# Kernel tuning notes

Hardware: AMD Instinct MI355X
Metric: run time of the kernel (lower is better)

## Reference

```python
import jax, jax.numpy as jnp
import numpy as np

C = 512
NH = 8
HD = C // NH
GROUPS = 8
EPS = 1e-5

def group_norm(x, w, b):
    # x: [B,C,H,W], 8 groups
    B, Cc, H, W = x.shape
    xg = x.reshape(B, GROUPS, Cc // GROUPS, H, W)
    mu = xg.mean(axis=(2, 3, 4), keepdims=True)
    var = xg.var(axis=(2, 3, 4), keepdims=True)
    xn = (xg - mu) * jax.lax.rsqrt(var + EPS)
    xn = xn.reshape(B, Cc, H, W)
    return xn * w[None, :, None, None] + b[None, :, None, None]

def conv1x1(x, w, b):
    # w: [O,C], b: [O]
    return jnp.einsum('oc,bchw->bohw', w, x) + b[None, :, None, None]

def setup_inputs() -> dict:
    key = jax.random.key(0)
    ks = jax.random.split(key, 12)
    s = 1.0 / np.sqrt(C)
    inp = {
        'x': jax.random.normal(ks[0], (8, C, 32, 32), dtype=jnp.float32),
        'norm_w': jnp.ones((C,), jnp.float32),
        'norm_b': jnp.zeros((C,), jnp.float32),
        'qw': jax.random.uniform(ks[1], (C, C), jnp.float32, -s, s),
        'qb': jax.random.uniform(ks[2], (C,), jnp.float32, -s, s),
        'kw': jax.random.uniform(ks[3], (C, C), jnp.float32, -s, s),
        'kb': jax.random.uniform(ks[4], (C,), jnp.float32, -s, s),
        'vw': jax.random.uniform(ks[5], (C, C), jnp.float32, -s, s),
        'vb': jax.random.uniform(ks[6], (C,), jnp.float32, -s, s),
        'pw': jax.random.uniform(ks[7], (C, C), jnp.float32, -s, s),
        'pb': jax.random.uniform(ks[8], (C,), jnp.float32, -s, s),
    }
    return inp

def reference(x, norm_w, norm_b, qw, qb, kw, kb, vw, vb, pw, pb):
    b, c, h, w = x.shape
    scale = HD ** (-0.5)
    xn = group_norm(x, norm_w, norm_b)
    q = conv1x1(xn, qw, qb).reshape(b, NH, HD, h * w)
    k = conv1x1(xn, kw, kb).reshape(b, NH, HD, h * w)
    v = conv1x1(xn, vw, vb).reshape(b, NH, HD, h * w)
    attn = jnp.einsum('bhcn,bhcm->bhnm', q, k) * scale
    attn = jax.nn.softmax(attn, axis=-1)
    out = jnp.einsum('bhnm,bhcm->bhcn', attn, v)
    out = out.reshape(b, c, h, w)
    out = conv1x1(out, pw, pb)
    return out + x
```

## Files before the change

kernel.cpp:

```cpp
#include <hip/hip_runtime.h>

#define C_DIM 512
#define N_PIX 1024
#define B_DIM 8
#define NHEAD 8
#define HDIM 64
#define NGRP 8
#define CG 64
#define EPSF 1e-5f

typedef __bf16 bf16x8_t __attribute__((ext_vector_type(8)));
typedef __bf16 bf16x4_t __attribute__((ext_vector_type(4)));
typedef float  f32x4_t  __attribute__((ext_vector_type(4)));
typedef unsigned int u32x4_t __attribute__((ext_vector_type(4)));

__device__ __forceinline__ __bf16 f2b(float f) {
  unsigned int u = __builtin_bit_cast(unsigned int, f);
  u += 0x7fffu + ((u >> 16) & 1u);
  unsigned short s = (unsigned short)(u >> 16);
  return __builtin_bit_cast(__bf16, s);
}

__device__ __forceinline__ unsigned int pack_trunc(float a, float b) {
  return (__builtin_bit_cast(unsigned int, a) >> 16) |
         (__builtin_bit_cast(unsigned int, b) & 0xffff0000u);
}

__device__ __forceinline__ void async16(const void* g, void* l) {
  __builtin_amdgcn_global_load_lds((const __attribute__((address_space(1))) void*)g,
                                   (__attribute__((address_space(3))) void*)l, 16, 0, 0);
}

__global__ __launch_bounds__(256) void prep_kernel(
    const float* __restrict__ qw, const float* __restrict__ kw,
    const float* __restrict__ vw, const float* __restrict__ pw,
    __bf16* __restrict__ wb,
    const float* __restrict__ x, float2* __restrict__ psum)
{
  if (blockIdx.x < 1024) {
    int idx = blockIdx.x * 256 + threadIdx.x;
    int mat = idx >> 16;
    int off = (idx & 65535) * 4;
    const float* src = (mat == 0) ? qw : (mat == 1) ? kw : (mat == 2) ? vw : pw;
    float4 v = *(const float4*)(src + off);
    bf16x4_t pk;
    pk[0] = f2b(v.x); pk[1] = f2b(v.y); pk[2] = f2b(v.z); pk[3] = f2b(v.w);
    *(bf16x4_t*)(wb + mat * (512 * 512) + off) = pk;
  } else {
    const int t = blockIdx.x - 1024;
    const int s = t & 7, bg = t >> 3;
    const float* xp = x + ((size_t)bg * CG + s * 8) * N_PIX;
    float sum = 0.f, sum2 = 0.f;
#pragma unroll
    for (int it = 0; it < 8; it++) {
      float4 v = ((const float4*)xp)[it * 256 + threadIdx.x];
      sum  += v.x + v.y + v.z + v.w;
      sum2 += v.x * v.x + v.y * v.y + v.z * v.z + v.w * v.w;
    }
#pragma unroll
    for (int off = 32; off; off >>= 1) {
      sum  += __shfl_xor(sum, off, 64);
      sum2 += __shfl_xor(sum2, off, 64);
    }
    __shared__ float red[8];
    const int lane = threadIdx.x & 63, wv = threadIdx.x >> 6;
    if (lane == 0) { red[wv] = sum; red[4 + wv] = sum2; }
    __syncthreads();
    if (threadIdx.x == 0) {
      float s1 = red[0] + red[1] + red[2] + red[3];
      float s2 = red[4] + red[5] + red[6] + red[7];
      psum[bg * 8 + s] = make_float2(s1, s2);
    }
  }
}

__global__ __launch_bounds__(256) void gn_apply_kernel(
    const float* __restrict__ x, const float2* __restrict__ psum,
    const float* __restrict__ gw, const float* __restrict__ gb,
    __bf16* __restrict__ xnT)
{
  const int n0 = blockIdx.x * 32, b = blockIdx.y;
  const int tid = threadIdx.x;
  __shared__ float mu_s[8], rs_s[8];
  __shared__ __align__(16) __bf16 tile[32 * 520];

  if (tid < 8) {
    float s1 = 0.f, s2 = 0.f;
#pragma unroll
    for (int i = 0; i < 8; i++) {
      float2 p = psum[(b * 8 + tid) * 8 + i];
      s1 += p.x; s2 += p.y;
    }
    const float inv = 1.f / (float)(CG * N_PIX);
    float mu = s1 * inv;
    float var = s2 * inv - mu * mu;
    mu_s[tid] = mu;
    rs_s[tid] = rsqrtf(var + EPSF);
  }
  __syncthreads();

  const float* xb = x + (size_t)b * C_DIM * N_PIX + n0;
  const int cl = tid >> 3;
  const int nq = (tid & 7) * 4;
#pragma unroll
  for (int co = 0; co < 16; co++) {
    const int c = co * 32 + cl;
    float4 v = *(const float4*)(xb + (size_t)c * N_PIX + nq);
    const int g = c >> 6;
    const float rs = rs_s[g];
    const float a = rs * gw[c];
    const float bb = gb[c] - mu_s[g] * a;
    tile[(nq + 0) * 520 + c] = f2b(v.x * a + bb);
    tile[(nq + 1) * 520 + c] = f2b(v.y * a + bb);
    tile[(nq + 2) * 520 + c] = f2b(v.z * a + bb);
    tile[(nq + 3) * 520 + c] = f2b(v.w * a + bb);
  }
  __syncthreads();

  __bf16* dst = xnT + ((size_t)b * N_PIX + n0) * C_DIM;
  const int l32 = tid & 31, nr = tid >> 5;
#pragma unroll
  for (int no = 0; no < 4; no++) {
    const int n = no * 8 + nr;
#pragma unroll
    for (int co = 0; co < 2; co++) {
      const int c = co * 256 + l32 * 8;
      *(bf16x8_t*)(dst + (size_t)n * C_DIM + c) =
          *(const bf16x8_t*)(tile + n * 520 + c);
    }
  }
}

__device__ __forceinline__ void gemm_core_64(
    const __bf16* __restrict__ A, const __bf16* __restrict__ B,
    __bf16* As, __bf16* Bs, f32x4_t acc[2][4])
{
  const int tid  = threadIdx.x;
  const int lane = tid & 63;
  const int wv   = tid >> 6;
  const int quad = lane >> 4;
  const int l16  = lane & 15;
  const int wm = (wv >> 1) * 32;
  const int wn = (wv & 1) * 64;

  f32x4_t zero = {0.f, 0.f, 0.f, 0.f};
#pragma unroll
  for (int i = 0; i < 2; i++)
#pragma unroll
    for (int j = 0; j < 4; j++) acc[i][j] = zero;

  const int chA  = wv * 64 + lane;
  const int rA = chA >> 2,  kA = (chA & 3) * 8;
  const int chB0 = wv * 64 + lane, chB1 = 256 + wv * 64 + lane;
  const int rB0 = chB0 >> 2, kB0 = (chB0 & 3) * 8;
  const int rB1 = chB1 >> 2, kB1 = (chB1 & 3) * 8;

  for (int kt = 0; kt < 512; kt += 64) {
#pragma unroll
    for (int p = 0; p < 2; p++) {
      async16(A + (size_t)rA * 512 + kt + p * 32 + kA,  As + p * 2048 + (wv * 64) * 8);
      async16(B + (size_t)rB0 * 512 + kt + p * 32 + kB0, Bs + p * 4096 + (wv * 64) * 8);
      async16(B + (size_t)rB1 * 512 + kt + p * 32 + kB1, Bs + p * 4096 + (256 + wv * 64) * 8);
    }
    __builtin_amdgcn_s_waitcnt(0);
    __syncthreads();
#pragma unroll
    for (int p = 0; p < 2; p++) {
      bf16x8_t af[2], bfr[4];
#pragma unroll
      for (int i = 0; i < 2; i++)
        af[i] = *(const bf16x8_t*)(As + p * 2048 + (wm + i * 16 + l16) * 32 + quad * 8);
#pragma unroll
      for (int j = 0; j < 4; j++)
        bfr[j] = *(const bf16x8_t*)(Bs + p * 4096 + (wn + j * 16 + l16) * 32 + quad * 8);
#pragma unroll
      for (int i = 0; i < 2; i++)
#pragma unroll
        for (int j = 0; j < 4; j++)
          acc[i][j] = __builtin_amdgcn_mfma_f32_16x16x32_bf16(af[i], bfr[j], acc[i][j], 0, 0, 0);
    }
    __syncthreads();
  }
}

__global__ __launch_bounds__(256, 4) void gemm_qkv_kernel(
    const __bf16* __restrict__ wqkv, const float* __restrict__ qb,
    const float* __restrict__ kb, const float* __restrict__ vb,
    const __bf16* __restrict__ xnT,
    __bf16* __restrict__ qT, __bf16* __restrict__ kT, __bf16* __restrict__ vbuf)
{
  __shared__ __align__(16) __bf16 smem[12288];
  __bf16* As = smem;
  __bf16* Bs = smem + 4096;
  const int b = blockIdx.x;
  const int n0 = blockIdx.y * 128;
  const int z = blockIdx.z;
  const int mat = z >> 3;
  const int m0 = (z & 7) * 64;
  const __bf16* A = wqkv + (size_t)mat * (512 * 512) + (size_t)m0 * 512;
  const __bf16* B = xnT + ((size_t)b * N_PIX + n0) * 512;
  f32x4_t acc[2][4];
  gemm_core_64(A, B, As, Bs, acc);

  const int tid = threadIdx.x, lane = tid & 63, wv = tid >> 6;
  const int quad = lane >> 4, l16 = lane & 15;
  const int wm = (wv >> 1) * 32, wn = (wv & 1) * 64;
  const float* bias = (mat == 0) ? qb : (mat == 1) ? kb : vb;
  const float qscale = (mat == 0) ? 0.125f * 1.44269504f : 1.0f;

  if (mat < 2) {
    __bf16* dst = (mat == 0) ? qT : kT;
#pragma unroll
    for (int i = 0; i < 2; i++) {
      const int crow = wm + i * 16 + quad * 4;
      const int o = m0 + crow;
      float b0 = bias[o], b1 = bias[o + 1], b2 = bias[o + 2], b3 = bias[o + 3];
#pragma unroll
      for (int j = 0; j < 4; j++) {
        const int nl = wn + j * 16 + l16;
        bf16x4_t pk;
        pk[0] = f2b((acc[i][j][0] + b0) * qscale);
        pk[1] = f2b((acc[i][j][1] + b1) * qscale);
        pk[2] = f2b((acc[i][j][2] + b2) * qscale);
        pk[3] = f2b((acc[i][j][3] + b3) * qscale);
        *(bf16x4_t*)(smem + nl * 72 + crow) = pk;
      }
    }
    __syncthreads();
#pragma unroll
    for (int it = 0; it < 4; it++) {
      const int n = it * 32 + (tid >> 3);
      const int c = (tid & 7) * 8;
      *(bf16x8_t*)(dst + ((size_t)b * N_PIX + n0 + n) * 512 + m0 + c) =
          *(const bf16x8_t*)(smem + n * 72 + c);
    }
  } else {
#pragma unroll
    for (int i = 0; i < 2; i++) {
      const int crow = wm + i * 16 + quad * 4;
      const int o = m0 + crow;
      float b0 = bias[o], b1 = bias[o + 1], b2 = bias[o + 2], b3 = bias[o + 3];
#pragma unroll
      for (int j = 0; j < 4; j++) {
        const int nl = wn + j * 16 + l16;
        smem[(crow + 0) * 132 + nl] = f2b(acc[i][j][0] + b0);
        smem[(crow + 1) * 132 + nl] = f2b(acc[i][j][1] + b1);
        smem[(crow + 2) * 132 + nl] = f2b(acc[i][j][2] + b2);
        smem[(crow + 3) * 132 + nl] = f2b(acc[i][j][3] + b3);
      }
    }
    __syncthreads();
    const int c = tid >> 2;
    const int nch = (tid & 3) * 32;
    __bf16* vd = vbuf + ((size_t)b * 512 + m0 + c) * N_PIX + n0 + nch;
#pragma unroll
    for (int k = 0; k < 4; k++)
      *(bf16x8_t*)(vd + k * 8) = *(const bf16x8_t*)(smem + c * 132 + nch + k * 8);
  }
}

__global__ __launch_bounds__(256, 2) void attn_kernel(
    const __bf16* __restrict__ qT, const __bf16* __restrict__ kT,
    const __bf16* __restrict__ vbuf, __bf16* __restrict__ aT)
{
  __shared__ __align__(16) __bf16 Ks[2][64 * 72];
  __shared__ __align__(16) __bf16 Vp[2][64 * 72];
  const int bh = blockIdx.x;
  const int b = bh >> 3, head = bh & 7;
  const int n0 = blockIdx.y * 128;
  const int tid = threadIdx.x, lane = tid & 63, wv = tid >> 6;
  const int quad = lane >> 4, l16 = lane & 15;

  bf16x8_t qf[2][2];
#pragma unroll
  for (int qt = 0; qt < 2; qt++) {
    const __bf16* qp = qT + ((size_t)b * N_PIX + n0 + wv * 32 + qt * 16 + l16) * 512 + head * 64;
    qf[qt][0] = *(const bf16x8_t*)(qp + quad * 8);
    qf[qt][1] = *(const bf16x8_t*)(qp + 32 + quad * 8);
  }

  const __bf16* kp = kT + ((size_t)b * N_PIX) * 512 + head * 64;
  const __bf16* vp = vbuf + ((size_t)b * 512 + head * 64) * N_PIX;

  const int srow = tid >> 2, scol = (tid & 3) * 16;
  const int pr0 = scol >> 5, hh0 = (scol >> 4) & 1;
  const int pos0 = pr0 * 32 + ((scol >> 2) & 3) * 8 + hh0 * 4;
  const int mc1 = scol + 8;
  const int pr1 = mc1 >> 5, hh1 = (mc1 >> 4) & 1;
  const int pos1 = pr1 * 32 + ((mc1 >> 2) & 3) * 8 + hh1 * 4;

  bf16x8_t kreg0 = *(const bf16x8_t*)(kp + (size_t)srow * 512 + scol);
  bf16x8_t kreg1 = *(const bf16x8_t*)(kp + (size_t)srow * 512 + scol + 8);
  bf16x8_t vreg0 = *(const bf16x8_t*)(vp + (size_t)srow * N_PIX + scol);
  bf16x8_t vreg1 = *(const bf16x8_t*)(vp + (size_t)srow * N_PIX + scol + 8);
  {
    *(bf16x8_t*)(Ks[0] + srow * 72 + scol)     = kreg0;
    *(bf16x8_t*)(Ks[0] + srow * 72 + scol + 8) = kreg1;
    bf16x4_t lo, hi;
#pragma unroll
    for (int r = 0; r < 4; r++) { lo[r] = vreg0[r]; hi[r] = vreg0[4 + r]; }
    *(bf16x4_t*)(Vp[0] + srow * 72 + pos0)     = lo;
    *(bf16x4_t*)(Vp[0] + srow * 72 + pos0 + 8) = hi;
#pragma unroll
    for (int r = 0; r < 4; r++) { lo[r] = vreg1[r]; hi[r] = vreg1[4 + r]; }
    *(bf16x4_t*)(Vp[0] + srow * 72 + pos1)     = lo;
    *(bf16x4_t*)(Vp[0] + srow * 72 + pos1 + 8) = hi;
  }
  kreg0 = *(const bf16x8_t*)(kp + (size_t)(64 + srow) * 512 + scol);
  kreg1 = *(const bf16x8_t*)(kp + (size_t)(64 + srow) * 512 + scol + 8);
  vreg0 = *(const bf16x8_t*)(vp + (size_t)srow * N_PIX + 64 + scol);
  vreg1 = *(const bf16x8_t*)(vp + (size_t)srow * N_PIX + 64 + scol + 8);
  __syncthreads();

  const f32x4_t zero = {0.f, 0.f, 0.f, 0.f};
  f32x4_t oacc[2][4];
#pragma unroll
  for (int qt = 0; qt < 2; qt++)
#pragma unroll
    for (int jc = 0; jc < 4; jc++) oacc[qt][jc] = zero;
  f32x4_t lsum4[2] = {zero, zero};

  for (int mt = 0; mt < 16; mt++) {
    const int cur = mt & 1, nxt = cur ^ 1;
    const __bf16* Kc = Ks[cur];
    const __bf16* Vc = Vp[cur];

    f32x4_t sacc[2][4];
#pragma unroll
    for (int mb = 0; mb < 4; mb++) {
      bf16x8_t kf0 = *(const bf16x8_t*)(Kc + (mb * 16 + l16) * 72 + quad * 8);
      bf16x8_t kf1 = *(const bf16x8_t*)(Kc + (mb * 16 + l16) * 72 + 32 + quad * 8);
#pragma unroll
      for (int qt = 0; qt < 2; qt++) {
        f32x4_t s = zero;
        s = __builtin_amdgcn_mfma_f32_16x16x32_bf16(kf0, qf[qt][0], s, 0, 0, 0);
        s = __builtin_amdgcn_mfma_f32_16x16x32_bf16(kf1, qf[qt][1], s, 0, 0, 0);
        sacc[qt][mb] = s;
      }
    }

    bf16x8_t pf[2][2];
#pragma unroll
    for (int qt = 0; qt < 2; qt++) {
      float p[4][4];
#pragma unroll
      for (int mb = 0; mb < 4; mb++)
#pragma unroll
        for (int r = 0; r < 4; r++) {
          p[mb][r] = __builtin_amdgcn_exp2f(sacc[qt][mb][r]);
          lsum4[qt][r] += p[mb][r];
        }
#pragma unroll
      for (int pr = 0; pr < 2; pr++) {
        u32x4_t u;
        u[0] = pack_trunc(p[2 * pr][0],     p[2 * pr][1]);
        u[1] = pack_trunc(p[2 * pr][2],     p[2 * pr][3]);
        u[2] = pack_trunc(p[2 * pr + 1][0], p[2 * pr + 1][1]);
        u[3] = pack_trunc(p[2 * pr + 1][2], p[2 * pr + 1][3]);
        pf[qt][pr] = __builtin_bit_cast(bf16x8_t, u);
      }
    }

#pragma unroll
    for (int jc = 0; jc < 4; jc++) {
      const int vrow = (jc * 16 + l16) * 72;
#pragma unroll
      for (int pr = 0; pr < 2; pr++) {
        bf16x8_t vf = *(const bf16x8_t*)(Vc + vrow + pr * 32 + quad * 8);
#pragma unroll
        for (int qt = 0; qt < 2; qt++)
          oacc[qt][jc] = __builtin_amdgcn_mfma_f32_16x16x32_bf16(vf, pf[qt][pr], oacc[qt][jc], 0, 0, 0);
      }
    }

    if (mt < 15) {
      *(bf16x8_t*)(Ks[nxt] + srow * 72 + scol)     = kreg0;
      *(bf16x8_t*)(Ks[nxt] + srow * 72 + scol + 8) = kreg1;
      bf16x4_t lo, hi;
#pragma unroll
      for (int r = 0; r < 4; r++) { lo[r] = vreg0[r]; hi[r] = vreg0[4 + r]; }
      *(bf16x4_t*)(Vp[nxt] + srow * 72 + pos0)     = lo;
      *(bf16x4_t*)(Vp[nxt] + srow * 72 + pos0 + 8) = hi;
#pragma unroll
      for (int r = 0; r < 4; r++) { lo[r] = vreg1[r]; hi[r] = vreg1[4 + r]; }
      *(bf16x4_t*)(Vp[nxt] + srow * 72 + pos1)     = lo;
      *(bf16x4_t*)(Vp[nxt] + srow * 72 + pos1 + 8) = hi;
      if (mt < 14) {
        kreg0 = *(const bf16x8_t*)(kp + (size_t)((mt + 2) * 64 + srow) * 512 + scol);
        kreg1 = *(const bf16x8_t*)(kp + (size_t)((mt + 2) * 64 + srow) * 512 + scol + 8);
        vreg0 = *(const bf16x8_t*)(vp + (size_t)srow * N_PIX + (mt + 2) * 64 + scol);
        vreg1 = *(const bf16x8_t*)(vp + (size_t)srow * N_PIX + (mt + 2) * 64 + scol + 8);
      }
      __syncthreads();
    }
  }

  __syncthreads();
  __bf16* Tr = &Ks[0][0];
#pragma unroll
  for (int qt = 0; qt < 2; qt++) {
    float lsum = lsum4[qt][0] + lsum4[qt][1] + lsum4[qt][2] + lsum4[qt][3];
    lsum += __shfl_xor(lsum, 16, 64);
    lsum += __shfl_xor(lsum, 32, 64);
    const float inv = 1.f / lsum;
    const int nl = wv * 32 + qt * 16 + l16;
#pragma unroll
    for (int jc = 0; jc < 4; jc++) {
      bf16x4_t o4;
#pragma unroll
      for (int r = 0; r < 4; r++) o4[r] = f2b(oacc[qt][jc][r] * inv);
      *(bf16x4_t*)(Tr + nl * 72 + jc * 16 + quad * 4) = o4;
    }
  }
  __syncthreads();
#pragma unroll
  for (int it = 0; it < 4; it++) {
    const int n = it * 32 + (tid >> 3);
    const int c = (tid & 7) * 8;
    *(bf16x8_t*)(aT + ((size_t)b * N_PIX + n0 + n) * 512 + head * 64 + c) =
        *(const bf16x8_t*)(Tr + n * 72 + c);
  }
}

__global__ __launch_bounds__(256, 4) void gemm_proj_kernel(
    const __bf16* __restrict__ wp, const float* __restrict__ pb,
    const __bf16* __restrict__ aT, const float* __restrict__ x,
    float* __restrict__ out)
{
  __shared__ __align__(16) __bf16 smem[12288];
  __bf16* As = smem;
  __bf16* Bs = smem + 4096;
  const int b = blockIdx.x;
  const int n0 = blockIdx.y * 128;
  const int m0 = blockIdx.z * 64;
  const __bf16* A = wp + (size_t)m0 * 512;
  const __bf16* B = aT + ((size_t)b * N_PIX + n0) * 512;
  f32x4_t acc[2][4];
  gemm_core_64(A, B, As, Bs, acc);
  const int tid = threadIdx.x, lane = tid & 63, wv = tid >> 6;
  const int quad = lane >> 4, l16 = lane & 15;
  const int wm = (wv >> 1) * 32, wn = (wv & 1) * 64;
#pragma unroll
  for (int i = 0; i < 2; i++) {
    const int o = m0 + wm + i * 16 + quad * 4;
#pragma unroll
    for (int j = 0; j < 4; j++) {
      const int n = n0 + wn + j * 16 + l16;
#pragma unroll
      for (int r = 0; r < 4; r++) {
        size_t idx = ((size_t)b * 512 + o + r) * N_PIX + n;
        out[idx] = acc[i][j][r] + pb[o + r] + x[idx];
      }
    }
  }
}

extern "C" void kernel_launch(void* const* d_in, const int* in_sizes, int n_in,
                              void* d_out, int out_size, void* d_ws, size_t ws_size,
                              hipStream_t stream)
{
  (void)in_sizes; (void)n_in; (void)out_size; (void)ws_size;
  const float* x   = (const float*)d_in[0];
  const float* gnw = (const float*)d_in[1];
  const float* gnb = (const float*)d_in[2];
  const float* qw  = (const float*)d_in[3];
  const float* qb  = (const float*)d_in[4];
  const float* kw  = (const float*)d_in[5];
  const float* kb  = (const float*)d_in[6];
  const float* vw  = (const float*)d_in[7];
  const float* vb  = (const float*)d_in[8];
  const float* pw  = (const float*)d_in[9];
  const float* pb  = (const float*)d_in[10];
  float* out = (float*)d_out;

  char* ws = (char*)d_ws;
  __bf16* wb   = (__bf16*)(ws);
  __bf16* xnT  = (__bf16*)(ws + (size_t)(2  << 20));
  __bf16* qTb  = (__bf16*)(ws + (size_t)(10 << 20));
  __bf16* kTb  = (__bf16*)(ws + (size_t)(18 << 20));
  __bf16* vbf  = (__bf16*)(ws + (size_t)(26 << 20));
  __bf16* aT   = (__bf16*)(ws + (size_t)(34 << 20));
  float2* psum = (float2*)(ws + (size_t)(42 << 20));

  hipLaunchKernelGGL(prep_kernel, dim3(1536), dim3(256), 0, stream,
                     qw, kw, vw, pw, wb, x, psum);
  hipLaunchKernelGGL(gn_apply_kernel, dim3(32, 8), dim3(256), 0, stream, x, psum, gnw, gnb, xnT);
  hipLaunchKernelGGL(gemm_qkv_kernel, dim3(8, 8, 24), dim3(256), 0, stream,
                     wb, qb, kb, vb, xnT, qTb, kTb, vbf);
  hipLaunchKernelGGL(attn_kernel, dim3(64, 8), dim3(256), 0, stream, qTb, kTb, vbf, aT);
  hipLaunchKernelGGL(gemm_proj_kernel, dim3(8, 8, 8), dim3(256), 0, stream,
                     wb + (size_t)3 * 512 * 512, pb, aT, x, out);
}
```

Before: 150.8 us.

## Fuse Q, K and V projections into one block sharing the activation tile

Each QKV GEMM block now computes the same 64-row output slice for all three weight matrices at once, so the xn activation tile is loaded once and reused across Q, K and V instead of being loaded three times by separate blocks. The grid shrinks from 1536 to 512 blocks, and each block holds three times the accumulators and a larger shared-memory buffer, with the occupancy bound lowered to 2. This cuts global and LDS traffic for the B operand but reduces parallelism to 512 blocks on a 256-CU device and raises register pressure.

```diff
diff --git a/kernel.cpp b/kernel.cpp
--- a/kernel.cpp
+++ b/kernel.cpp
@@ -183,32 +183,79 @@
   }
 }
 
-__global__ __launch_bounds__(256, 4) void gemm_qkv_kernel(
+__global__ __launch_bounds__(256, 2) void gemm_qkv_kernel(
     const __bf16* __restrict__ wqkv, const float* __restrict__ qb,
     const float* __restrict__ kb, const float* __restrict__ vb,
     const __bf16* __restrict__ xnT,
     __bf16* __restrict__ qT, __bf16* __restrict__ kT, __bf16* __restrict__ vbuf)
 {
-  __shared__ __align__(16) __bf16 smem[12288];
-  __bf16* As = smem;
-  __bf16* Bs = smem + 4096;
+  __shared__ __align__(16) __bf16 smem[20480];
+  __bf16* Bs = smem + 12288;
   const int b = blockIdx.x;
   const int n0 = blockIdx.y * 128;
-  const int z = blockIdx.z;
-  const int mat = z >> 3;
-  const int m0 = (z & 7) * 64;
-  const __bf16* A = wqkv + (size_t)mat * (512 * 512) + (size_t)m0 * 512;
-  const __bf16* B = xnT + ((size_t)b * N_PIX + n0) * 512;
-  f32x4_t acc[2][4];
-  gemm_core_64(A, B, As, Bs, acc);
+  const int m0 = blockIdx.z * 64;
+  const __bf16* Aq = wqkv + (size_t)m0 * 512;
+  const __bf16* Ak = Aq + 512 * 512;
+  const __bf16* Av = Ak + 512 * 512;
+  const __bf16* Bx = xnT + ((size_t)b * N_PIX + n0) * 512;
 
   const int tid = threadIdx.x, lane = tid & 63, wv = tid >> 6;
   const int quad = lane >> 4, l16 = lane & 15;
   const int wm = (wv >> 1) * 32, wn = (wv & 1) * 64;
-  const float* bias = (mat == 0) ? qb : (mat == 1) ? kb : vb;
-  const float qscale = (mat == 0) ? 0.125f * 1.44269504f : 1.0f;
-
-  if (mat < 2) {
+
+  const f32x4_t zero = {0.f, 0.f, 0.f, 0.f};
+  f32x4_t acc[3][2][4];
+#pragma unroll
+  for (int m = 0; m < 3; m++)
+#pragma unroll
+    for (int i = 0; i < 2; i++)
+#pragma unroll
+      for (int j = 0; j < 4; j++) acc[m][i][j] = zero;
+
+  const int chA = wv * 64 + lane;
+  const int rA = chA >> 2, kA = (chA & 3) * 8;
+  const int chB0 = wv * 64 + lane, chB1 = 256 + wv * 64 + lane;
+  const int rB0 = chB0 >> 2, kB0 = (chB0 & 3) * 8;
+  const int rB1 = chB1 >> 2, kB1 = (chB1 & 3) * 8;
+
+  for (int kt = 0; kt < 512; kt += 64) {
+#pragma unroll
+    for (int p = 0; p < 2; p++) {
+      async16(Aq + (size_t)rA * 512 + kt + p * 32 + kA, smem + p * 2048 + (wv * 64) * 8);
+      async16(Ak + (size_t)rA * 512 + kt + p * 32 + kA, smem + 4096 + p * 2048 + (wv * 64) * 8);
+      async16(Av + (size_t)rA * 512 + kt + p * 32 + kA, smem + 8192 + p * 2048 + (wv * 64) * 8);
+      async16(Bx + (size_t)rB0 * 512 + kt + p * 32 + kB0, Bs + p * 4096 + (wv * 64) * 8);
+      async16(Bx + (size_t)rB1 * 512 + kt + p * 32 + kB1, Bs + p * 4096 + (256 + wv * 64) * 8);
+    }
+    __builtin_amdgcn_s_waitcnt(0);
+    __syncthreads();
+#pragma unroll
+    for (int p = 0; p < 2; p++) {
+      bf16x8_t bfr[4];
+#pragma unroll
+      for (int j = 0; j < 4; j++)
+        bfr[j] = *(const bf16x8_t*)(Bs + p * 4096 + (wn + j * 16 + l16) * 32 + quad * 8);
+#pragma unroll
+      for (int m = 0; m < 3; m++) {
+        bf16x8_t af[2];
+#pragma unroll
+        for (int i = 0; i < 2; i++)
+          af[i] = *(const bf16x8_t*)(smem + m * 4096 + p * 2048 + (wm + i * 16 + l16) * 32 + quad * 8);
+#pragma unroll
+        for (int i = 0; i < 2; i++)
+#pragma unroll
+          for (int j = 0; j < 4; j++)
+            acc[m][i][j] = __builtin_amdgcn_mfma_f32_16x16x32_bf16(af[i], bfr[j], acc[m][i][j], 0, 0, 0);
+      }
+    }
+    __syncthreads();
+  }
+
+  const float qscale = 0.125f * 1.44269504f;
+#pragma unroll
+  for (int mat = 0; mat < 2; mat++) {
+    const float* bias = (mat == 0) ? qb : kb;
+    const float sc = (mat == 0) ? qscale : 1.0f;
     __bf16* dst = (mat == 0) ? qT : kT;
 #pragma unroll
     for (int i = 0; i < 2; i++) {
@@ -219,10 +266,10 @@
       for (int j = 0; j < 4; j++) {
         const int nl = wn + j * 16 + l16;
         bf16x4_t pk;
-        pk[0] = f2b((acc[i][j][0] + b0) * qscale);
-        pk[1] = f2b((acc[i][j][1] + b1) * qscale);
-        pk[2] = f2b((acc[i][j][2] + b2) * qscale);
-        pk[3] = f2b((acc[i][j][3] + b3) * qscale);
+        pk[0] = f2b((acc[mat][i][j][0] + b0) * sc);
+        pk[1] = f2b((acc[mat][i][j][1] + b1) * sc);
+        pk[2] = f2b((acc[mat][i][j][2] + b2) * sc);
+        pk[3] = f2b((acc[mat][i][j][3] + b3) * sc);
         *(bf16x4_t*)(smem + nl * 72 + crow) = pk;
       }
     }
@@ -234,22 +281,24 @@
       *(bf16x8_t*)(dst + ((size_t)b * N_PIX + n0 + n) * 512 + m0 + c) =
           *(const bf16x8_t*)(smem + n * 72 + c);
     }
-  } else {
-#pragma unroll
-    for (int i = 0; i < 2; i++) {
-      const int crow = wm + i * 16 + quad * 4;
-      const int o = m0 + crow;
-      float b0 = bias[o], b1 = bias[o + 1], b2 = bias[o + 2], b3 = bias[o + 3];
-#pragma unroll
-      for (int j = 0; j < 4; j++) {
-        const int nl = wn + j * 16 + l16;
-        smem[(crow + 0) * 132 + nl] = f2b(acc[i][j][0] + b0);
-        smem[(crow + 1) * 132 + nl] = f2b(acc[i][j][1] + b1);
-        smem[(crow + 2) * 132 + nl] = f2b(acc[i][j][2] + b2);
-        smem[(crow + 3) * 132 + nl] = f2b(acc[i][j][3] + b3);
-      }
-    }
-    __syncthreads();
+    __syncthreads();
+  }
+#pragma unroll
+  for (int i = 0; i < 2; i++) {
+    const int crow = wm + i * 16 + quad * 4;
+    const int o = m0 + crow;
+    float b0 = vb[o], b1 = vb[o + 1], b2 = vb[o + 2], b3 = vb[o + 3];
+#pragma unroll
+    for (int j = 0; j < 4; j++) {
+      const int nl = wn + j * 16 + l16;
+      smem[(crow + 0) * 132 + nl] = f2b(acc[2][i][j][0] + b0);
+      smem[(crow + 1) * 132 + nl] = f2b(acc[2][i][j][1] + b1);
+      smem[(crow + 2) * 132 + nl] = f2b(acc[2][i][j][2] + b2);
+      smem[(crow + 3) * 132 + nl] = f2b(acc[2][i][j][3] + b3);
+    }
+  }
+  __syncthreads();
+  {
     const int c = tid >> 2;
     const int nch = (tid & 3) * 32;
     __bf16* vd = vbuf + ((size_t)b * 512 + m0 + c) * N_PIX + n0 + nch;
@@ -485,7 +534,7 @@
   hipLaunchKernelGGL(prep_kernel, dim3(1536), dim3(256), 0, stream,
                      qw, kw, vw, pw, wb, x, psum);
   hipLaunchKernelGGL(gn_apply_kernel, dim3(32, 8), dim3(256), 0, stream, x, psum, gnw, gnb, xnT);
-  hipLaunchKernelGGL(gemm_qkv_kernel, dim3(8, 8, 24), dim3(256), 0, stream,
+  hipLaunchKernelGGL(gemm_qkv_kernel, dim3(8, 8, 8), dim3(256), 0, stream,
                      wb, qb, kb, vb, xnT, qTb, kTb, vbf);
   hipLaunchKernelGGL(attn_kernel, dim3(64, 8), dim3(256), 0, stream, qTb, kTb, vbf, aT);
   hipLaunchKernelGGL(gemm_proj_kernel, dim3(8, 8, 8), dim3(256), 0, stream,
```

After: 149.5 us. Within noise of the previous version (-0.9%).
